# Performance work log

Hardware: AMD Instinct MI355X
Metric: run time of the kernel (lower is better)

Reference implementation:

```python
import jax, jax.numpy as jnp
import numpy as np

B, L, D, K = 16, 2048, 128, 8192
NUM_RQ_STEPS = 1


def _nearest(residual, codebook):
    # residual: [B,L,D], codebook: [K,D]
    d2 = (
        jnp.sum(residual * residual, axis=-1, keepdims=True)  # [B,L,1]
        - 2.0 * jnp.einsum('bld,kd->blk', residual, codebook)  # [B,L,K]
        + jnp.sum(codebook * codebook, axis=-1)  # [K]
    )
    idx = jnp.argmin(d2, axis=-1)  # [B,L]
    return codebook[idx], idx  # gather: [B,L,D]


def setup_inputs() -> dict:
    key = jax.random.key(0)
    k1, k2 = jax.random.split(key)
    z_e = jax.random.normal(k1, (B, L, D), dtype=jnp.float32)
    codebook = jax.random.normal(k2, (K, D), dtype=jnp.float32)
    return {"z_e": z_e, "codebook": codebook}


def reference(z_e, codebook):
    # apply_codebook(z_e, code_sg=True): codebook is stop-gradiented,
    # residual quantization over NUM_RQ_STEPS, straight-through on output.
    cb = jax.lax.stop_gradient(codebook)
    residual = z_e
    z_q = jnp.zeros_like(z_e)
    idx_list = []
    for _ in range(NUM_RQ_STEPS):
        q, idx = _nearest(residual, cb)
        z_q = z_q + q
        residual = residual - q
        idx_list.append(idx)
    indices = jnp.stack(idx_list, axis=-1)  # [B,L,num_rq_steps]
    # straight-through estimator (code_sg=True): grads flow to z_e, not codebook
    z_q = z_e + jax.lax.stop_gradient(z_q - z_e)
    return z_q, indices
```

## Files before the change

### kernel.cpp

```cpp
#include <hip/hip_runtime.h>


#define M_TOK  32768
#define DIM    128
#define KCODES 8192
#define BM     64
#define NT     (KCODES / 256)
#define MARGIN 3e-4f

typedef _Float16 half8v __attribute__((ext_vector_type(8)));
typedef float float4v __attribute__((ext_vector_type(4)));

union H2U { _Float16 h; unsigned short u; };
__device__ __forceinline__ unsigned short f2h_bits(_Float16 h) {
  H2U c; c.h = h; return c.u;
}

__device__ __forceinline__ void gload_lds16(const void* g, void* l) {
  __builtin_amdgcn_global_load_lds(
      (const __attribute__((address_space(1))) unsigned int*)g,
      (__attribute__((address_space(3))) unsigned int*)l, 16, 0, 0);
}

__device__ __forceinline__ unsigned int fmap(float f) {
  union { float f; unsigned int u; } c; c.f = f;
  return (c.u >> 31) ? ~c.u : (c.u | 0x80000000u);
}

#define CNORM_OFF  (KCODES * 512)
#define QCNT_OFF   (CNORM_OFF + KCODES * 4)
#define QTOK_OFF   (QCNT_OFF + 64)
#define KMIN_OFF   (QTOK_OFF + M_TOK * 4)

__global__ __launch_bounds__(256) void prep_kernel(
    const float* __restrict__ cb, unsigned short* __restrict__ Cs,
    float* __restrict__ cnorm, int* __restrict__ qcnt) {
  if (blockIdx.x == 0 && threadIdx.x == 0) *qcnt = 0;
  const int k = blockIdx.x * 4 + (threadIdx.x >> 6);
  const int lane = threadIdx.x & 63;
  const float2 v = ((const float2*)(cb + (size_t)k * DIM))[lane];
  float s = v.x * v.x + v.y * v.y;
  #pragma unroll
  for (int off = 32; off > 0; off >>= 1) s += __shfl_down(s, off);
  if (lane == 0) cnorm[k] = s;
  const _Float16 hx = (_Float16)v.x, hy = (_Float16)v.y;
  ushort2 hi, lo;
  hi.x = f2h_bits(hx); hi.y = f2h_bits(hy);
  lo.x = f2h_bits((_Float16)(v.x - (float)hx));
  lo.y = f2h_bits((_Float16)(v.y - (float)hy));
  *(ushort2*)(Cs + (size_t)k * 256 + lane * 2) = hi;
  *(ushort2*)(Cs + (size_t)k * 256 + 128 + lane * 2) = lo;
}

__global__ __launch_bounds__(256, 2) void vq_mfma_kernel(
    const float* __restrict__ ze, const unsigned short* __restrict__ Cs,
    const float* __restrict__ cnorm, const float* __restrict__ cb,
    int* __restrict__ qcnt, int* __restrict__ qtok,
    unsigned long long* __restrict__ kmin,
    float* __restrict__ out_zq, float* __restrict__ out_idx) {
  __shared__ char lds[49152];
  char* const As = lds;
  char* const Bs = lds + 32768;

  const int tid = threadIdx.x;
  const int wn = tid >> 6;
  const int lane = tid & 63;
  const int quad = lane >> 4;
  const int l15 = lane & 15;
  const int m0 = blockIdx.x * BM;

  int loffC[4];
  #pragma unroll
  for (int c = 0; c < 4; ++c) {
    const int r = c * 16 + (lane >> 2);
    const int s = lane & 3;
    const int seg = s ^ ((r >> 1) & 3);
    loffC[c] = (wn * 64 + r) * 512 + seg * 16;
  }
  int boff[4];
  #pragma unroll
  for (int j = 0; j < 4; ++j) {
    const int n = j * 16 + l15;
    boff[j] = n * 64 + ((quad ^ ((n >> 1) & 3)) << 4);
  }
  char* const BsW = Bs + wn * 4096;

  {
    const int r = tid >> 2;
    const int qh = tid & 3;
    const float* zrow = ze + (size_t)(m0 + r) * DIM + qh * 32;
    char* arow = As + r * 512;
    const int rx = r & 7;
    #pragma unroll
    for (int i = 0; i < 8; ++i) {
      const float4 v = *(const float4*)(zrow + i * 4);
      const _Float16 h0 = (_Float16)v.x, h1 = (_Float16)v.y,
                     h2 = (_Float16)v.z, h3 = (_Float16)v.w;
      ushort4 hh, ll;
      hh.x = f2h_bits(h0); hh.y = f2h_bits(h1);
      hh.z = f2h_bits(h2); hh.w = f2h_bits(h3);
      ll.x = f2h_bits((_Float16)(v.x - (float)h0));
      ll.y = f2h_bits((_Float16)(v.y - (float)h1));
      ll.z = f2h_bits((_Float16)(v.z - (float)h2));
      ll.w = f2h_bits((_Float16)(v.w - (float)h3));
      const int c = qh * 32 + i * 4;
      *(ushort4*)(arow + ((((c >> 3) ^ rx) << 4) | ((c & 7) << 1))) = hh;
      const int c2 = c + 128;
      *(ushort4*)(arow + ((((c2 >> 3) ^ rx) << 4) | ((c2 & 7) << 1))) = ll;
    }
  }
  __syncthreads();

  half8v ahi[4][4];
  #pragma unroll
  for (int ks = 0; ks < 4; ++ks)
    #pragma unroll
    for (int i = 0; i < 4; ++i) {
      const int m = i * 16 + l15;
      const int kslot = ks * 4 + quad;
      ahi[ks][i] = *(const half8v*)(As + m * 512 + ((kslot ^ (m & 7)) << 4));
    }

  float bestv[16], secv[16], idxv[16];
  #pragma unroll
  for (int s = 0; s < 16; ++s) {
    bestv[s] = 3.4e38f; secv[s] = 3.4e38f; idxv[s] = 0.f;
  }

  for (int nt = 0; nt < NT; ++nt) {
    const char* const tile = (const char*)Cs + (size_t)nt * 131072;
    float cnv[4];
    #pragma unroll
    for (int j = 0; j < 4; ++j)
      cnv[j] = cnorm[nt * 256 + wn * 64 + j * 16 + l15];

    float4v acc[4][4];
    #pragma unroll
    for (int i = 0; i < 4; ++i)
      #pragma unroll
      for (int j = 0; j < 4; ++j) acc[i][j] = (float4v)0.0f;

    #pragma unroll
    for (int kk = 0; kk < 8; ++kk) {
      __syncthreads();
      #pragma unroll
      for (int c = 0; c < 4; ++c)
        gload_lds16(tile + kk * 64 + loffC[c], BsW + c * 1024);
      __syncthreads();

      half8v bf[4];
      #pragma unroll
      for (int j = 0; j < 4; ++j) bf[j] = *(const half8v*)(BsW + boff[j]);

      if (kk < 4) {
        #pragma unroll
        for (int i = 0; i < 4; ++i)
          #pragma unroll
          for (int j = 0; j < 4; ++j)
            acc[i][j] = __builtin_amdgcn_mfma_f32_16x16x32_f16(
                ahi[kk][i], bf[j], acc[i][j], 0, 0, 0);
        half8v alo[4];
        #pragma unroll
        for (int i = 0; i < 4; ++i) {
          const int m = i * 16 + l15;
          const int kslot = 16 + kk * 4 + quad;
          alo[i] = *(const half8v*)(As + m * 512 + ((kslot ^ (m & 7)) << 4));
        }
        #pragma unroll
        for (int i = 0; i < 4; ++i)
          #pragma unroll
          for (int j = 0; j < 4; ++j)
            acc[i][j] = __builtin_amdgcn_mfma_f32_16x16x32_f16(
                alo[i], bf[j], acc[i][j], 0, 0, 0);
      } else {
        #pragma unroll
        for (int i = 0; i < 4; ++i)
          #pragma unroll
          for (int j = 0; j < 4; ++j)
            acc[i][j] = __builtin_amdgcn_mfma_f32_16x16x32_f16(
                ahi[kk - 4][i], bf[j], acc[i][j], 0, 0, 0);
      }
    }

    #pragma unroll
    for (int j = 0; j < 4; ++j) {
      const float nidx = (float)(nt * 256 + wn * 64 + j * 16 + l15);
      const float cn = cnv[j];
      #pragma unroll
      for (int i = 0; i < 4; ++i)
        #pragma unroll
        for (int rg = 0; rg < 4; ++rg) {
          const float sc = fmaf(-2.0f, acc[i][j][rg], cn);
          const int slot = i * 4 + rg;
          const bool bt = sc < bestv[slot];
          secv[slot] = bt ? bestv[slot] : fminf(secv[slot], sc);
          idxv[slot] = bt ? nidx : idxv[slot];
          bestv[slot] = bt ? sc : bestv[slot];
        }
    }
  }

  #pragma unroll
  for (int slot = 0; slot < 16; ++slot) {
    float b = bestv[slot], sec = secv[slot], ix = idxv[slot];
    #pragma unroll
    for (int mk = 1; mk <= 8; mk <<= 1) {
      const float ob = __shfl_xor(b, mk);
      const float os = __shfl_xor(sec, mk);
      const float oi = __shfl_xor(ix, mk);
      const bool take = (ob < b) || (ob == b && oi < ix);
      const float loser = take ? b : ob;
      b = take ? ob : b;
      ix = take ? oi : ix;
      sec = fminf(fminf(sec, os), loser);
    }
    bestv[slot] = b; secv[slot] = sec; idxv[slot] = ix;
  }

  __syncthreads();
  float* const redB = (float*)lds;
  float* const redS = redB + 256;
  float* const redI = redB + 512;
  float* const lidxs = redB + 768;
  if (l15 == 0) {
    #pragma unroll
    for (int slot = 0; slot < 16; ++slot) {
      const int row = (slot >> 2) * 16 + quad * 4 + (slot & 3);
      redB[wn * 64 + row] = bestv[slot];
      redS[wn * 64 + row] = secv[slot];
      redI[wn * 64 + row] = idxv[slot];
    }
  }
  __syncthreads();
  if (tid < 64) {
    float b = redB[tid], sec = redS[tid], ix = redI[tid];
    #pragma unroll
    for (int w = 1; w < 4; ++w) {
      const float ob = redB[w * 64 + tid];
      const float os = redS[w * 64 + tid];
      const float oi = redI[w * 64 + tid];
      const bool take = (ob < b) || (ob == b && oi < ix);
      const float loser = take ? b : ob;
      b = take ? ob : b;
      ix = take ? oi : ix;
      sec = fminf(fminf(sec, os), loser);
    }
    out_idx[m0 + tid] = ix;
    lidxs[tid] = ix;
    if (sec - b < MARGIN) {
      kmin[m0 + tid] = ~0ull;
      const int p = atomicAdd(qcnt, 1);
      qtok[p] = m0 + tid;
    }
  }
  __syncthreads();

  const int tl = tid >> 2, qp = tid & 3;
  const int code = (int)lidxs[tl];
  const float4* src = (const float4*)(cb + (size_t)code * DIM);
  float4* dst = (float4*)(out_zq + (size_t)(m0 + tl) * DIM);
  #pragma unroll
  for (int p = 0; p < 8; ++p) dst[qp + p * 4] = src[qp + p * 4];
}

__global__ __launch_bounds__(256) void rescan_part_kernel(
    const float* __restrict__ ze, const float* __restrict__ cb,
    const float* __restrict__ cnorm, const int* __restrict__ qcnt,
    const int* __restrict__ qtok, unsigned long long* __restrict__ kmin) {
  __shared__ float xsh[DIM];
  __shared__ float rs[256];
  __shared__ int ri[256];
  const int tid = threadIdx.x;
  const int chunk = blockIdx.x & 31;
  const int n = *qcnt;
  for (int qi = blockIdx.x >> 5; qi < n; qi += (gridDim.x >> 5)) {
    const int token = qtok[qi];
    __syncthreads();
    if (tid < 32)
      ((float4*)xsh)[tid] = ((const float4*)(ze + (size_t)token * DIM))[tid];
    __syncthreads();
    const int code = chunk * 256 + tid;
    const float* crow = cb + (size_t)code * DIM;
    float dot = 0.f;
    #pragma unroll
    for (int d = 0; d < DIM; ++d) dot = fmaf(xsh[d], crow[d], dot);
    rs[tid] = fmaf(-2.f, dot, cnorm[code]);
    ri[tid] = code;
    __syncthreads();
    #pragma unroll
    for (int off = 128; off > 0; off >>= 1) {
      if (tid < off) {
        const float so = rs[tid + off];
        const int io = ri[tid + off];
        if (so < rs[tid] || (so == rs[tid] && io < ri[tid])) {
          rs[tid] = so; ri[tid] = io;
        }
      }
      __syncthreads();
    }
    if (tid == 0) {
      union { float f; unsigned int u; } c; c.f = rs[0];
      const unsigned int m = (c.u >> 31) ? ~c.u : (c.u | 0x80000000u);
      const unsigned long long key =
          ((unsigned long long)m << 32) | (unsigned int)ri[0];
      atomicMin(&kmin[token], key);
    }
    __syncthreads();
  }
}

__global__ __launch_bounds__(256) void rescan_apply_kernel(
    const float* __restrict__ cb, const int* __restrict__ qcnt,
    const int* __restrict__ qtok, const unsigned long long* __restrict__ kmin,
    float* __restrict__ out_zq, float* __restrict__ out_idx) {
  const int tid = threadIdx.x;
  const int n = *qcnt;
  for (int qi = blockIdx.x; qi < n; qi += gridDim.x) {
    const int token = qtok[qi];
    const int code = (int)(unsigned int)(kmin[token] & 0xFFFFFFFFull);
    if (tid == 0) out_idx[token] = (float)code;
    if (tid < 32)
      ((float4*)(out_zq + (size_t)token * DIM))[tid] =
          ((const float4*)(cb + (size_t)code * DIM))[tid];
  }
}

extern "C" void kernel_launch(void* const* d_in, const int* in_sizes, int n_in,
                              void* d_out, int out_size, void* d_ws,
                              size_t ws_size, hipStream_t stream) {
  const float* ze = (const float*)d_in[0];
  const float* cb = (const float*)d_in[1];
  float* out = (float*)d_out;

  unsigned short* Cs = (unsigned short*)d_ws;
  float* cnorm = (float*)((char*)d_ws + CNORM_OFF);
  int* qcnt = (int*)((char*)d_ws + QCNT_OFF);
  int* qtok = (int*)((char*)d_ws + QTOK_OFF);
  unsigned long long* kmin = (unsigned long long*)((char*)d_ws + KMIN_OFF);

  prep_kernel<<<KCODES / 4, 256, 0, stream>>>(cb, Cs, cnorm, qcnt);
  vq_mfma_kernel<<<M_TOK / BM, 256, 0, stream>>>(
      ze, Cs, cnorm, cb, qcnt, qtok, kmin, out, out + (size_t)M_TOK * DIM);
  rescan_part_kernel<<<4096, 256, 0, stream>>>(ze, cb, cnorm, qcnt, qtok,
                                               kmin);
  rescan_apply_kernel<<<256, 256, 0, stream>>>(cb, qcnt, qtok, kmin, out,
                                               out + (size_t)M_TOK * DIM);
}
```

Baseline: 284.6 us.

## Drop split-fp16 low terms and widen margin for exact rescoring

```diff
diff --git a/kernel.cpp b/kernel.cpp
--- a/kernel.cpp
+++ b/kernel.cpp
@@ -6,7 +6,7 @@
 #define KCODES 8192
 #define BM     64
 #define NT     (KCODES / 256)
-#define MARGIN 3e-4f
+#define MARGIN 0.10f
 
 typedef _Float16 half8v __attribute__((ext_vector_type(8)));
 typedef float float4v __attribute__((ext_vector_type(4)));
@@ -22,12 +22,7 @@
       (__attribute__((address_space(3))) unsigned int*)l, 16, 0, 0);
 }
 
-__device__ __forceinline__ unsigned int fmap(float f) {
-  union { float f; unsigned int u; } c; c.f = f;
-  return (c.u >> 31) ? ~c.u : (c.u | 0x80000000u);
-}
-
-#define CNORM_OFF  (KCODES * 512)
+#define CNORM_OFF  (KCODES * 256)
 #define QCNT_OFF   (CNORM_OFF + KCODES * 4)
 #define QTOK_OFF   (QCNT_OFF + 64)
 #define KMIN_OFF   (QTOK_OFF + M_TOK * 4)
@@ -43,13 +38,10 @@
   #pragma unroll
   for (int off = 32; off > 0; off >>= 1) s += __shfl_down(s, off);
   if (lane == 0) cnorm[k] = s;
-  const _Float16 hx = (_Float16)v.x, hy = (_Float16)v.y;
-  ushort2 hi, lo;
-  hi.x = f2h_bits(hx); hi.y = f2h_bits(hy);
-  lo.x = f2h_bits((_Float16)(v.x - (float)hx));
-  lo.y = f2h_bits((_Float16)(v.y - (float)hy));
-  *(ushort2*)(Cs + (size_t)k * 256 + lane * 2) = hi;
-  *(ushort2*)(Cs + (size_t)k * 256 + 128 + lane * 2) = lo;
+  ushort2 hi;
+  hi.x = f2h_bits((_Float16)v.x);
+  hi.y = f2h_bits((_Float16)v.y);
+  *(ushort2*)(Cs + (size_t)k * 128 + lane * 2) = hi;
 }
 
 __global__ __launch_bounds__(256, 2) void vq_mfma_kernel(
@@ -60,7 +52,7 @@
     float* __restrict__ out_zq, float* __restrict__ out_idx) {
   __shared__ char lds[49152];
   char* const As = lds;
-  char* const Bs = lds + 32768;
+  char* const Bs = lds + 16384;
 
   const int tid = threadIdx.x;
   const int wn = tid >> 6;
@@ -75,7 +67,7 @@
     const int r = c * 16 + (lane >> 2);
     const int s = lane & 3;
     const int seg = s ^ ((r >> 1) & 3);
-    loffC[c] = (wn * 64 + r) * 512 + seg * 16;
+    loffC[c] = (wn * 64 + r) * 256 + seg * 16;
   }
   int boff[4];
   #pragma unroll
@@ -83,30 +75,24 @@
     const int n = j * 16 + l15;
     boff[j] = n * 64 + ((quad ^ ((n >> 1) & 3)) << 4);
   }
-  char* const BsW = Bs + wn * 4096;
+  char* const BsW = Bs + wn * 8192;
 
   {
     const int r = tid >> 2;
     const int qh = tid & 3;
     const float* zrow = ze + (size_t)(m0 + r) * DIM + qh * 32;
-    char* arow = As + r * 512;
+    char* arow = As + r * 256;
     const int rx = r & 7;
     #pragma unroll
     for (int i = 0; i < 8; ++i) {
       const float4 v = *(const float4*)(zrow + i * 4);
-      const _Float16 h0 = (_Float16)v.x, h1 = (_Float16)v.y,
-                     h2 = (_Float16)v.z, h3 = (_Float16)v.w;
-      ushort4 hh, ll;
-      hh.x = f2h_bits(h0); hh.y = f2h_bits(h1);
-      hh.z = f2h_bits(h2); hh.w = f2h_bits(h3);
-      ll.x = f2h_bits((_Float16)(v.x - (float)h0));
-      ll.y = f2h_bits((_Float16)(v.y - (float)h1));
-      ll.z = f2h_bits((_Float16)(v.z - (float)h2));
-      ll.w = f2h_bits((_Float16)(v.w - (float)h3));
+      ushort4 hh;
+      hh.x = f2h_bits((_Float16)v.x);
+      hh.y = f2h_bits((_Float16)v.y);
+      hh.z = f2h_bits((_Float16)v.z);
+      hh.w = f2h_bits((_Float16)v.w);
       const int c = qh * 32 + i * 4;
       *(ushort4*)(arow + ((((c >> 3) ^ rx) << 4) | ((c & 7) << 1))) = hh;
-      const int c2 = c + 128;
-      *(ushort4*)(arow + ((((c2 >> 3) ^ rx) << 4) | ((c2 & 7) << 1))) = ll;
     }
   }
   __syncthreads();
@@ -118,7 +104,7 @@
     for (int i = 0; i < 4; ++i) {
       const int m = i * 16 + l15;
       const int kslot = ks * 4 + quad;
-      ahi[ks][i] = *(const half8v*)(As + m * 512 + ((kslot ^ (m & 7)) << 4));
+      ahi[ks][i] = *(const half8v*)(As + m * 256 + ((kslot ^ (m & 7)) << 4));
     }
 
   float bestv[16], secv[16], idxv[16];
@@ -128,7 +114,7 @@
   }
 
   for (int nt = 0; nt < NT; ++nt) {
-    const char* const tile = (const char*)Cs + (size_t)nt * 131072;
+    const char* const tile = (const char*)Cs + (size_t)nt * 65536;
     float cnv[4];
     #pragma unroll
     for (int j = 0; j < 4; ++j)
@@ -141,44 +127,29 @@
       for (int j = 0; j < 4; ++j) acc[i][j] = (float4v)0.0f;
 
     #pragma unroll
-    for (int kk = 0; kk < 8; ++kk) {
+    for (int t = 0; t < 2; ++t) {
       __syncthreads();
       #pragma unroll
-      for (int c = 0; c < 4; ++c)
-        gload_lds16(tile + kk * 64 + loffC[c], BsW + c * 1024);
+      for (int p = 0; p < 2; ++p)
+        #pragma unroll
+        for (int c = 0; c < 4; ++c)
+          gload_lds16(tile + (t * 2 + p) * 64 + loffC[c],
+                      BsW + p * 4096 + c * 1024);
       __syncthreads();
 
-      half8v bf[4];
       #pragma unroll
-      for (int j = 0; j < 4; ++j) bf[j] = *(const half8v*)(BsW + boff[j]);
-
-      if (kk < 4) {
+      for (int p = 0; p < 2; ++p) {
+        const int kk = t * 2 + p;
+        half8v bf[4];
+        #pragma unroll
+        for (int j = 0; j < 4; ++j)
+          bf[j] = *(const half8v*)(BsW + p * 4096 + boff[j]);
         #pragma unroll
         for (int i = 0; i < 4; ++i)
           #pragma unroll
           for (int j = 0; j < 4; ++j)
             acc[i][j] = __builtin_amdgcn_mfma_f32_16x16x32_f16(
                 ahi[kk][i], bf[j], acc[i][j], 0, 0, 0);
-        half8v alo[4];
-        #pragma unroll
-        for (int i = 0; i < 4; ++i) {
-          const int m = i * 16 + l15;
-          const int kslot = 16 + kk * 4 + quad;
-          alo[i] = *(const half8v*)(As + m * 512 + ((kslot ^ (m & 7)) << 4));
-        }
-        #pragma unroll
-        for (int i = 0; i < 4; ++i)
-          #pragma unroll
-          for (int j = 0; j < 4; ++j)
-            acc[i][j] = __builtin_amdgcn_mfma_f32_16x16x32_f16(
-                alo[i], bf[j], acc[i][j], 0, 0, 0);
-      } else {
-        #pragma unroll
-        for (int i = 0; i < 4; ++i)
-          #pragma unroll
-          for (int j = 0; j < 4; ++j)
-            acc[i][j] = __builtin_amdgcn_mfma_f32_16x16x32_f16(
-                ahi[kk - 4][i], bf[j], acc[i][j], 0, 0, 0);
       }
     }
 
```

New measurement: 269.1 us. 1.06x faster.
